# Performance work log

Hardware: AMD Instinct MI355X
Metric: run time of the kernel (lower is better)

The kernel has to match this reference:

```python
import jax, jax.numpy as jnp
import numpy as np
from jax import lax

T, B, DX, H, DZ = 512, 64, 128, 256, 64
W_SCALE = 0.05


def setup_inputs() -> dict:
    key = jax.random.key(0)
    ks = jax.random.split(key, 16)
    r = lambda k, shape, s=W_SCALE: jax.random.normal(k, shape, dtype=jnp.float32) * s
    return {
        "X": jax.random.normal(ks[0], (T, B, DX), dtype=jnp.float32),
        "Wih_f": r(ks[1], (H, DX)), "Whh_f": r(ks[2], (H, H)),
        "bih_f": r(ks[3], (H,)), "bhh_f": r(ks[4], (H,)),
        "Wih_b": r(ks[5], (H, DX)), "Whh_b": r(ks[6], (H, H)),
        "bih_b": r(ks[7], (H,)), "bhh_b": r(ks[8], (H,)),
        "Wt": r(ks[9], (H, DZ)), "bt": r(ks[10], (H,)),
        "Wmu": r(ks[11], (DZ, H)), "bmu": r(ks[12], (DZ,)),
        "Wsig": r(ks[13], (DZ, H)), "bsig": r(ks[14], (DZ,)),
        "eps": jax.random.normal(ks[15], (T, B, DZ), dtype=jnp.float32),
    }


def _rnn_dir(X, Wih, Whh, bih, bhh):
    # Elman RNN (tanh): h_t = tanh(x_t Wih^T + bih + h_{t-1} Whh^T + bhh)
    xproj = jnp.einsum('tbd,hd->tbh', X, Wih) + bih + bhh  # big GEMM hoisted out of scan

    def step(h, xp):
        h = jnp.tanh(xp + h @ Whh.T)
        return h, h

    h0 = jnp.zeros((X.shape[1], Whh.shape[0]), dtype=X.dtype)
    _, hs = lax.scan(step, h0, xproj)
    return hs  # [T,B,H]


def reference(X, Wih_f, Whh_f, bih_f, bhh_f, Wih_b, Whh_b, bih_b, bhh_b,
              Wt, bt, Wmu, bmu, Wsig, bsig, eps):
    h_left = _rnn_dir(X, Wih_f, Whh_f, bih_f, bhh_f)
    h_right = _rnn_dir(X[::-1], Wih_b, Whh_b, bih_b, bhh_b)[::-1]

    def step(z_prev, inputs):
        hl, hr, eps_t = inputs
        tmp = jnp.tanh(z_prev @ Wt.T + bt)           # transition_net
        h_t = (tmp + hl + hr) * (1.0 / 3.0)
        mu = h_t @ Wmu.T + bmu
        std = jax.nn.softplus(h_t @ Wsig.T + bsig)
        z = mu + std * eps_t                         # reparameterization
        return z, (z, mu, std)

    z0 = jnp.zeros((X.shape[1], Wt.shape[1]), dtype=X.dtype)
    _, (z, mu, std) = lax.scan(step, z0, (h_left, h_right, eps))
    # stack outputs {z_post, mu_post, std_post} into one array [3,T,B,DZ]
    return jnp.stack([z, mu, std])
```

## Files before the change

### kernel.cpp

```cpp
#include <hip/hip_runtime.h>

#define TT 512
#define BB 64
#define DXX 128
#define HH 256
#define DZZ 64

typedef __attribute__((ext_vector_type(8))) short short8;
typedef __attribute__((ext_vector_type(4))) float f32x4;

#define DEV static __device__ __forceinline__

DEV unsigned short f2bf(float f){
  unsigned u = __builtin_bit_cast(unsigned, f);
  u += 0x7FFFu + ((u >> 16) & 1u);
  return (unsigned short)(u >> 16);
}
DEV float bf2f(unsigned short s){
  unsigned u = ((unsigned)s) << 16;
  return __builtin_bit_cast(float, u);
}
DEV float ftanh(float x){
  float a = fabsf(x);
  float e = __expf(-2.f * a);
  float r = __builtin_amdgcn_rcpf(1.f + e);
  float t = (1.f - e) * r;
  return copysignf(t, x);
}
DEV float fsoftplus(float x){
  float e = __expf(fminf(x, 20.f));
  float s = __logf(1.f + e);
  return (x > 20.f) ? x : s;
}
DEV short8 pack8(const float* p){
  short8 v;
  #pragma unroll
  for (int i = 0; i < 8; ++i) v[i] = (short)f2bf(p[i]);
  return v;
}


__global__ __launch_bounds__(256, 2) void phaseA(
    const float* __restrict__ X,
    const float* __restrict__ WihF, const float* __restrict__ bihF, const float* __restrict__ bhhF,
    const float* __restrict__ WihB, const float* __restrict__ bihB, const float* __restrict__ bhhB,
    unsigned short* __restrict__ xpF)
{
  const int bid = blockIdx.x;
  const int d = bid >> 9, s = bid & 511;
  const int ts = d ? (TT - 1 - s) : s;
  const float* W  = d ? WihB : WihF;
  const float* bi = d ? bihB : bihF;
  const float* bh = d ? bhhB : bhhF;

  const int tid = threadIdx.x, q = tid >> 6, l = tid & 63;
  const int l15 = l & 15, l4 = l >> 4;

  short8 bfv[4][4];
  float bias[4];
  #pragma unroll
  for (int ni = 0; ni < 4; ++ni){
    int n = 64*q + 16*ni + l15;
    bias[ni] = bi[n] + bh[n];
    #pragma unroll
    for (int ks = 0; ks < 4; ++ks)
      bfv[ni][ks] = pack8(W + (size_t)n * DXX + ks*32 + l4*8);
  }

  #pragma unroll
  for (int bq = 0; bq < 4; ++bq){
    const float* xr = X + ((size_t)ts * 64 + 16*bq + l15) * DXX;
    short8 af[4];
    #pragma unroll
    for (int ks = 0; ks < 4; ++ks) af[ks] = pack8(xr + ks*32 + l4*8);

    f32x4 acc[4];
    #pragma unroll
    for (int ni = 0; ni < 4; ++ni){
      acc[ni][0]=bias[ni]; acc[ni][1]=bias[ni]; acc[ni][2]=bias[ni]; acc[ni][3]=bias[ni];
    }
    #pragma unroll
    for (int ks = 0; ks < 4; ++ks)
      #pragma unroll
      for (int ni = 0; ni < 4; ++ni)
        acc[ni] = __builtin_amdgcn_mfma_f32_16x16x32_bf16(af[ks], bfv[ni][ks], acc[ni], 0, 0, 0);

    unsigned wd[8];
    #pragma unroll
    for (int w8 = 0; w8 < 8; ++w8){
      int ni = w8 >> 1, rb = (w8 & 1) * 2;
      wd[w8] = (unsigned)f2bf(acc[ni][rb]) | ((unsigned)f2bf(acc[ni][rb+1]) << 16);
    }
    unsigned short* dst = xpF + ((((size_t)d*TT + s)*4 + bq)*4 + q)*1024 + (size_t)l*16;
    uint4 o0 = {wd[0], wd[1], wd[2], wd[3]};
    uint4 o1 = {wd[4], wd[5], wd[6], wd[7]};
    ((uint4*)dst)[0] = o0;
    ((uint4*)dst)[1] = o1;
  }
}

__global__ void epsPerm(const float* __restrict__ eps, float* __restrict__ epsF){
  const int t = blockIdx.x, tid = threadIdx.x;
  const int q = tid >> 6, l = tid & 63;
  const int l15 = l & 15, l4 = l >> 4;
  const int nz = 16*q + l15;
  #pragma unroll
  for (int bq = 0; bq < 4; ++bq){
    float4 o;
    int m0 = 16*bq + l4*4;
    o.x = eps[((size_t)t*64 + m0 + 0)*64 + nz];
    o.y = eps[((size_t)t*64 + m0 + 1)*64 + nz];
    o.z = eps[((size_t)t*64 + m0 + 2)*64 + nz];
    o.w = eps[((size_t)t*64 + m0 + 3)*64 + nz];
    *(float4*)(epsF + ((((size_t)t*4 + bq)*4 + q)*64 + l)*4) = o;
  }
}

__global__ __launch_bounds__(256, 1) void phaseB(
    const float* __restrict__ WhhF, const float* __restrict__ WhhB,
    const unsigned short* __restrict__ xpF, unsigned short* __restrict__ hF)
{
  const int dir = blockIdx.x >> 2, bq = blockIdx.x & 3;
  const float* Whh = dir ? WhhB : WhhF;
  const int tid = threadIdx.x, q = tid >> 6, l = tid & 63;
  const int l15 = l & 15, l4 = l >> 4;

  __shared__ __attribute__((aligned(16))) unsigned short hbuf[2][16 * 256];

  short8 bf[4][8];
  #pragma unroll
  for (int ni = 0; ni < 4; ++ni){
    int n = 64*q + 16*ni + l15;
    #pragma unroll
    for (int ks = 0; ks < 8; ++ks)
      bf[ni][ks] = pack8(Whh + (size_t)n * HH + ks*32 + l4*8);
  }
  for (int i = tid; i < 16*256/2; i += 256) ((unsigned*)hbuf[0])[i] = 0u;

  const size_t strideS = 16384;
  const size_t laneOff = (size_t)bq*4096 + (size_t)q*1024 + (size_t)l*16;
  const unsigned short* xpP = xpF + (size_t)dir*TT*strideS + laneOff;
  unsigned short* hD = hF + (size_t)dir*TT*strideS + laneOff;

  uint4 xq0, xq1;
  { const uint4* src = (const uint4*)xpP; xq0 = src[0]; xq1 = src[1]; }

  unsigned pw[8];
  size_t prevOff = 0;
  __syncthreads();

  for (int s = 0; s < TT; ++s){
    if (s > 0){
      uint4 o0 = {pw[0], pw[1], pw[2], pw[3]};
      uint4 o1 = {pw[4], pw[5], pw[6], pw[7]};
      *(uint4*)(hD + prevOff)     = o0;
      *(uint4*)(hD + prevOff + 8) = o1;
    }
    const int rp = s & 1, wc = rp ^ 1;

    f32x4 acc[4];
    {
      unsigned w8v[8] = {xq0.x, xq0.y, xq0.z, xq0.w, xq1.x, xq1.y, xq1.z, xq1.w};
      #pragma unroll
      for (int w8 = 0; w8 < 8; ++w8){
        int ni = w8 >> 1, rb = (w8 & 1) * 2;
        acc[ni][rb]   = bf2f((unsigned short)(w8v[w8] & 0xffff));
        acc[ni][rb+1] = bf2f((unsigned short)(w8v[w8] >> 16));
      }
    }
    if (s + 1 < TT){
      const uint4* src = (const uint4*)(xpP + (size_t)(s+1) * strideS);
      xq0 = src[0]; xq1 = src[1];
    }
    #pragma unroll
    for (int ks = 0; ks < 8; ++ks){
      int idx = (l15*256 + ks*32 + l4*8) ^ ((l15 & 7) << 3);
      short8 a = *(const short8*)(hbuf[rp] + idx);
      #pragma unroll
      for (int ni = 0; ni < 4; ++ni)
        acc[ni] = __builtin_amdgcn_mfma_f32_16x16x32_bf16(a, bf[ni][ks], acc[ni], 0, 0, 0);
    }
    #pragma unroll
    for (int ni = 0; ni < 4; ++ni){
      int n = 64*q + 16*ni + l15;
      #pragma unroll
      for (int rb = 0; rb < 4; rb += 2){
        unsigned u0 = f2bf(ftanh(acc[ni][rb]));
        unsigned u1 = f2bf(ftanh(acc[ni][rb+1]));
        int m0 = l4*4 + rb, m1 = m0 + 1;
        hbuf[wc][(m0*256 + n) ^ ((m0 & 7) << 3)] = (unsigned short)u0;
        hbuf[wc][(m1*256 + n) ^ ((m1 & 7) << 3)] = (unsigned short)u1;
        pw[ni*2 + (rb >> 1)] = u0 | (u1 << 16);
      }
    }
    prevOff = (size_t)(dir ? (TT - 1 - s) : s) * strideS;
    __syncthreads();
  }
  {
    uint4 o0 = {pw[0], pw[1], pw[2], pw[3]};
    uint4 o1 = {pw[4], pw[5], pw[6], pw[7]};
    *(uint4*)(hD + prevOff)     = o0;
    *(uint4*)(hD + prevOff + 8) = o1;
  }
}

__global__ __launch_bounds__(256, 1) void phaseC(
    const float* __restrict__ Wt,  const float* __restrict__ bt,
    const float* __restrict__ Wmu, const float* __restrict__ bmu,
    const float* __restrict__ Wsig,const float* __restrict__ bsig,
    const float* __restrict__ epsF, const unsigned short* __restrict__ hF,
    float* __restrict__ out)
{
  const int bq = blockIdx.x;
  const int tid = threadIdx.x, q = tid >> 6, l = tid & 63;
  const int l15 = l & 15, l4 = l >> 4;

  __shared__ __attribute__((aligned(16))) unsigned short zbuf[16 * 64];
  __shared__ __attribute__((aligned(16))) unsigned short hbuf[16 * 256];

  short8 btf[4][2]; float btr[4];
  #pragma unroll
  for (int ni = 0; ni < 4; ++ni){
    int n = 64*q + 16*ni + l15;
    btr[ni] = bt[n];
    #pragma unroll
    for (int ks = 0; ks < 2; ++ks)
      btf[ni][ks] = pack8(Wt + (size_t)n * DZZ + ks*32 + l4*8);
  }
  short8 bmsf[2][8]; float bms[2];
  {
    int r = 16*q + l15;
    bms[0] = bmu[r]; bms[1] = bsig[r];
    #pragma unroll
    for (int ks = 0; ks < 8; ++ks){
      bmsf[0][ks] = pack8(Wmu  + (size_t)r * HH + ks*32 + l4*8);
      bmsf[1][ks] = pack8(Wsig + (size_t)r * HH + ks*32 + l4*8);
    }
  }
  for (int i = tid; i < 16*64/2; i += 256) ((unsigned*)zbuf)[i] = 0u;

  const size_t strideS = 16384;
  const size_t laneOff = (size_t)bq*4096 + (size_t)q*1024 + (size_t)l*16;
  const unsigned short* hLp = hF + laneOff;
  const unsigned short* hRp = hLp + (size_t)TT * strideS;
  const float* eP = epsF + (((size_t)bq*4 + q)*64 + l)*4;

  unsigned hlw[8], hrw[8];
  float efv[4];
  {
    const uint4* sl = (const uint4*)hLp;
    const uint4* sr = (const uint4*)hRp;
    uint4 a = sl[0], b = sl[1], c = sr[0], d2 = sr[1];
    hlw[0]=a.x; hlw[1]=a.y; hlw[2]=a.z; hlw[3]=a.w; hlw[4]=b.x; hlw[5]=b.y; hlw[6]=b.z; hlw[7]=b.w;
    hrw[0]=c.x; hrw[1]=c.y; hrw[2]=c.z; hrw[3]=c.w; hrw[4]=d2.x; hrw[5]=d2.y; hrw[6]=d2.z; hrw[7]=d2.w;
    float4 e4 = *(const float4*)eP;
    efv[0]=e4.x; efv[1]=e4.y; efv[2]=e4.z; efv[3]=e4.w;
  }
  const size_t TBZ = (size_t)TT * 64 * 64;
  const int nz = 16*q + l15;
  float dmu[4], dsp[4], dz[4];

  __syncthreads();

  for (int t = 0; t < TT; ++t){
    if (t > 0){
      #pragma unroll
      for (int reg = 0; reg < 4; ++reg){
        int M = 16*bq + l4*4 + reg;
        size_t ob = ((size_t)(t-1)*64 + M)*64 + nz;
        out[ob]         = dz[reg];
        out[TBZ + ob]   = dmu[reg];
        out[2*TBZ + ob] = dsp[reg];
      }
    }
    f32x4 at[4];
    #pragma unroll
    for (int ni = 0; ni < 4; ++ni){
      at[ni][0]=btr[ni]; at[ni][1]=btr[ni]; at[ni][2]=btr[ni]; at[ni][3]=btr[ni];
    }
    #pragma unroll
    for (int ks = 0; ks < 2; ++ks){
      int idx = (l15*64 + ks*32 + l4*8) ^ ((l15 & 7) << 3);
      short8 a = *(const short8*)(zbuf + idx);
      #pragma unroll
      for (int ni = 0; ni < 4; ++ni)
        at[ni] = __builtin_amdgcn_mfma_f32_16x16x32_bf16(a, btf[ni][ks], at[ni], 0, 0, 0);
    }
    #pragma unroll
    for (int ni = 0; ni < 4; ++ni){
      int n = 64*q + 16*ni + l15;
      #pragma unroll
      for (int rb = 0; rb < 4; rb += 2){
        unsigned lw = hlw[ni*2 + (rb >> 1)], rw = hrw[ni*2 + (rb >> 1)];
        float h0 = (ftanh(at[ni][rb])   + bf2f((unsigned short)(lw & 0xffff)) + bf2f((unsigned short)(rw & 0xffff))) * (1.f/3.f);
        float h1 = (ftanh(at[ni][rb+1]) + bf2f((unsigned short)(lw >> 16))    + bf2f((unsigned short)(rw >> 16)))    * (1.f/3.f);
        int m0 = l4*4 + rb, m1 = m0 + 1;
        hbuf[(m0*256 + n) ^ ((m0 & 7) << 3)] = f2bf(h0);
        hbuf[(m1*256 + n) ^ ((m1 & 7) << 3)] = f2bf(h1);
      }
    }
    if (t + 1 < TT){
      const uint4* sl = (const uint4*)(hLp + (size_t)(t+1)*strideS);
      const uint4* sr = (const uint4*)(hRp + (size_t)(t+1)*strideS);
      uint4 a = sl[0], b = sl[1], c = sr[0], d2 = sr[1];
      hlw[0]=a.x; hlw[1]=a.y; hlw[2]=a.z; hlw[3]=a.w; hlw[4]=b.x; hlw[5]=b.y; hlw[6]=b.z; hlw[7]=b.w;
      hrw[0]=c.x; hrw[1]=c.y; hrw[2]=c.z; hrw[3]=c.w; hrw[4]=d2.x; hrw[5]=d2.y; hrw[6]=d2.z; hrw[7]=d2.w;
    }
    __syncthreads();

    f32x4 am[2];
    am[0][0]=bms[0]; am[0][1]=bms[0]; am[0][2]=bms[0]; am[0][3]=bms[0];
    am[1][0]=bms[1]; am[1][1]=bms[1]; am[1][2]=bms[1]; am[1][3]=bms[1];
    #pragma unroll
    for (int ks = 0; ks < 8; ++ks){
      int idx = (l15*256 + ks*32 + l4*8) ^ ((l15 & 7) << 3);
      short8 a = *(const short8*)(hbuf + idx);
      am[0] = __builtin_amdgcn_mfma_f32_16x16x32_bf16(a, bmsf[0][ks], am[0], 0, 0, 0);
      am[1] = __builtin_amdgcn_mfma_f32_16x16x32_bf16(a, bmsf[1][ks], am[1], 0, 0, 0);
    }
    #pragma unroll
    for (int reg = 0; reg < 4; ++reg){
      float mu = am[0][reg];
      float sp = fsoftplus(am[1][reg]);
      float zv = mu + sp * efv[reg];
      int m = l4*4 + reg;
      zbuf[(m*64 + nz) ^ ((m & 7) << 3)] = f2bf(zv);
      dmu[reg] = mu; dsp[reg] = sp; dz[reg] = zv;
    }
    if (t + 1 < TT){
      float4 e4 = *(const float4*)(eP + (size_t)(t+1)*4096);
      efv[0]=e4.x; efv[1]=e4.y; efv[2]=e4.z; efv[3]=e4.w;
    }
    __syncthreads();
  }
  {
    #pragma unroll
    for (int reg = 0; reg < 4; ++reg){
      int M = 16*bq + l4*4 + reg;
      size_t ob = ((size_t)(TT-1)*64 + M)*64 + nz;
      out[ob]         = dz[reg];
      out[TBZ + ob]   = dmu[reg];
      out[2*TBZ + ob] = dsp[reg];
    }
  }
}

extern "C" void kernel_launch(void* const* d_in, const int* in_sizes, int n_in,
                              void* d_out, int out_size, void* d_ws, size_t ws_size,
                              hipStream_t stream)
{
  const float* X      = (const float*)d_in[0];
  const float* Wih_f  = (const float*)d_in[1];
  const float* Whh_f  = (const float*)d_in[2];
  const float* bih_f  = (const float*)d_in[3];
  const float* bhh_f  = (const float*)d_in[4];
  const float* Wih_b  = (const float*)d_in[5];
  const float* Whh_b  = (const float*)d_in[6];
  const float* bih_b  = (const float*)d_in[7];
  const float* bhh_b  = (const float*)d_in[8];
  const float* Wt     = (const float*)d_in[9];
  const float* bt     = (const float*)d_in[10];
  const float* Wmu    = (const float*)d_in[11];
  const float* bmu    = (const float*)d_in[12];
  const float* Wsig   = (const float*)d_in[13];
  const float* bsig   = (const float*)d_in[14];
  const float* eps    = (const float*)d_in[15];

  unsigned short* xpF = (unsigned short*)d_ws;
  unsigned short* hF  = xpF + (size_t)2 * TT * 16384;
  float* epsF = (float*)(hF + (size_t)2 * TT * 16384);

  phaseA<<<dim3(1024), dim3(256), 0, stream>>>(X, Wih_f, bih_f, bhh_f, Wih_b, bih_b, bhh_b, xpF);
  epsPerm<<<dim3(512), dim3(256), 0, stream>>>(eps, epsF);
  phaseB<<<dim3(8), dim3(256), 0, stream>>>(Whh_f, Whh_b, xpF, hF);
  phaseC<<<dim3(4), dim3(256), 0, stream>>>(Wt, bt, Wmu, bmu, Wsig, bsig, epsF, hF, (float*)d_out);
}
```

Measured before the change: 1.214 ms.

## Swap MFMA operand order to transpose accumulator layout and drop eps permute kernel

```diff
diff --git a/kernel.cpp b/kernel.cpp
--- a/kernel.cpp
+++ b/kernel.cpp
@@ -16,10 +16,11 @@
   u += 0x7FFFu + ((u >> 16) & 1u);
   return (unsigned short)(u >> 16);
 }
-DEV float bf2f(unsigned short s){
-  unsigned u = ((unsigned)s) << 16;
-  return __builtin_bit_cast(float, u);
-}
+DEV unsigned pack2(float lo, float hi){
+  return (unsigned)f2bf(lo) | ((unsigned)f2bf(hi) << 16);
+}
+DEV float bfLO(unsigned u){ return __builtin_bit_cast(float, u << 16); }
+DEV float bfHI(unsigned u){ return __builtin_bit_cast(float, u & 0xffff0000u); }
 DEV float ftanh(float x){
   float a = fabsf(x);
   float e = __expf(-2.f * a);
@@ -56,63 +57,47 @@
   const int tid = threadIdx.x, q = tid >> 6, l = tid & 63;
   const int l15 = l & 15, l4 = l >> 4;
 
-  short8 bfv[4][4];
-  float bias[4];
+  short8 wf[4][4];
+  f32x4 bias[4];
   #pragma unroll
   for (int ni = 0; ni < 4; ++ni){
     int n = 64*q + 16*ni + l15;
-    bias[ni] = bi[n] + bh[n];
     #pragma unroll
     for (int ks = 0; ks < 4; ++ks)
-      bfv[ni][ks] = pack8(W + (size_t)n * DXX + ks*32 + l4*8);
+      wf[ni][ks] = pack8(W + (size_t)n * DXX + ks*32 + l4*8);
+    int n0 = 64*q + 16*ni + 4*l4;
+    float4 b1 = *(const float4*)(bi + n0);
+    float4 b2 = *(const float4*)(bh + n0);
+    bias[ni][0]=b1.x+b2.x; bias[ni][1]=b1.y+b2.y; bias[ni][2]=b1.z+b2.z; bias[ni][3]=b1.w+b2.w;
   }
 
   #pragma unroll
   for (int bq = 0; bq < 4; ++bq){
     const float* xr = X + ((size_t)ts * 64 + 16*bq + l15) * DXX;
-    short8 af[4];
-    #pragma unroll
-    for (int ks = 0; ks < 4; ++ks) af[ks] = pack8(xr + ks*32 + l4*8);
+    short8 xf[4];
+    #pragma unroll
+    for (int ks = 0; ks < 4; ++ks) xf[ks] = pack8(xr + ks*32 + l4*8);
 
     f32x4 acc[4];
     #pragma unroll
+    for (int ni = 0; ni < 4; ++ni) acc[ni] = bias[ni];
+    #pragma unroll
+    for (int ks = 0; ks < 4; ++ks)
+      #pragma unroll
+      for (int ni = 0; ni < 4; ++ni)
+        acc[ni] = __builtin_amdgcn_mfma_f32_16x16x32_bf16(wf[ni][ks], xf[ks], acc[ni], 0, 0, 0);
+
+    unsigned wd[8];
+    #pragma unroll
     for (int ni = 0; ni < 4; ++ni){
-      acc[ni][0]=bias[ni]; acc[ni][1]=bias[ni]; acc[ni][2]=bias[ni]; acc[ni][3]=bias[ni];
-    }
-    #pragma unroll
-    for (int ks = 0; ks < 4; ++ks)
-      #pragma unroll
-      for (int ni = 0; ni < 4; ++ni)
-        acc[ni] = __builtin_amdgcn_mfma_f32_16x16x32_bf16(af[ks], bfv[ni][ks], acc[ni], 0, 0, 0);
-
-    unsigned wd[8];
-    #pragma unroll
-    for (int w8 = 0; w8 < 8; ++w8){
-      int ni = w8 >> 1, rb = (w8 & 1) * 2;
-      wd[w8] = (unsigned)f2bf(acc[ni][rb]) | ((unsigned)f2bf(acc[ni][rb+1]) << 16);
+      wd[ni*2]   = pack2(acc[ni][0], acc[ni][1]);
+      wd[ni*2+1] = pack2(acc[ni][2], acc[ni][3]);
     }
     unsigned short* dst = xpF + ((((size_t)d*TT + s)*4 + bq)*4 + q)*1024 + (size_t)l*16;
     uint4 o0 = {wd[0], wd[1], wd[2], wd[3]};
     uint4 o1 = {wd[4], wd[5], wd[6], wd[7]};
     ((uint4*)dst)[0] = o0;
     ((uint4*)dst)[1] = o1;
-  }
-}
-
-__global__ void epsPerm(const float* __restrict__ eps, float* __restrict__ epsF){
-  const int t = blockIdx.x, tid = threadIdx.x;
-  const int q = tid >> 6, l = tid & 63;
-  const int l15 = l & 15, l4 = l >> 4;
-  const int nz = 16*q + l15;
-  #pragma unroll
-  for (int bq = 0; bq < 4; ++bq){
-    float4 o;
-    int m0 = 16*bq + l4*4;
-    o.x = eps[((size_t)t*64 + m0 + 0)*64 + nz];
-    o.y = eps[((size_t)t*64 + m0 + 1)*64 + nz];
-    o.z = eps[((size_t)t*64 + m0 + 2)*64 + nz];
-    o.w = eps[((size_t)t*64 + m0 + 3)*64 + nz];
-    *(float4*)(epsF + ((((size_t)t*4 + bq)*4 + q)*64 + l)*4) = o;
   }
 }
 
@@ -124,18 +109,20 @@
   const float* Whh = dir ? WhhB : WhhF;
   const int tid = threadIdx.x, q = tid >> 6, l = tid & 63;
   const int l15 = l & 15, l4 = l >> 4;
-
-  __shared__ __attribute__((aligned(16))) unsigned short hbuf[2][16 * 256];
-
-  short8 bf[4][8];
+  const int swz = (l15 & 7) << 3;
+  const int rbase = l15 * 256;
+
+  __shared__ __attribute__((aligned(16))) unsigned short hbuf[2][4096];
+
+  short8 wf[4][8];
   #pragma unroll
   for (int ni = 0; ni < 4; ++ni){
     int n = 64*q + 16*ni + l15;
     #pragma unroll
     for (int ks = 0; ks < 8; ++ks)
-      bf[ni][ks] = pack8(Whh + (size_t)n * HH + ks*32 + l4*8);
-  }
-  for (int i = tid; i < 16*256/2; i += 256) ((unsigned*)hbuf[0])[i] = 0u;
+      wf[ni][ks] = pack8(Whh + (size_t)n * HH + ks*32 + l4*8);
+  }
+  for (int i = tid; i < 2048; i += 256) ((unsigned*)hbuf[0])[i] = 0u;
 
   const size_t strideS = 16384;
   const size_t laneOff = (size_t)bq*4096 + (size_t)q*1024 + (size_t)l*16;
@@ -145,204 +132,201 @@
   uint4 xq0, xq1;
   { const uint4* src = (const uint4*)xpP; xq0 = src[0]; xq1 = src[1]; }
 
-  unsigned pw[8];
+  uint4 p0, p1;
   size_t prevOff = 0;
   __syncthreads();
 
   for (int s = 0; s < TT; ++s){
     if (s > 0){
-      uint4 o0 = {pw[0], pw[1], pw[2], pw[3]};
-      uint4 o1 = {pw[4], pw[5], pw[6], pw[7]};
-      *(uint4*)(hD + prevOff)     = o0;
-      *(uint4*)(hD + prevOff + 8) = o1;
-    }
-    const int rp = s & 1, wc = rp ^ 1;
-
+      *(uint4*)(hD + prevOff)     = p0;
+      *(uint4*)(hD + prevOff + 8) = p1;
+    }
+    uint4 xn0, xn1;
+    {
+      int sn = (s + 1 < TT) ? s + 1 : s;
+      const uint4* src = (const uint4*)(xpP + (size_t)sn * strideS);
+      xn0 = src[0]; xn1 = src[1];
+    }
     f32x4 acc[4];
     {
-      unsigned w8v[8] = {xq0.x, xq0.y, xq0.z, xq0.w, xq1.x, xq1.y, xq1.z, xq1.w};
-      #pragma unroll
-      for (int w8 = 0; w8 < 8; ++w8){
-        int ni = w8 >> 1, rb = (w8 & 1) * 2;
-        acc[ni][rb]   = bf2f((unsigned short)(w8v[w8] & 0xffff));
-        acc[ni][rb+1] = bf2f((unsigned short)(w8v[w8] >> 16));
+      unsigned W8[8] = {xq0.x, xq0.y, xq0.z, xq0.w, xq1.x, xq1.y, xq1.z, xq1.w};
+      #pragma unroll
+      for (int ni = 0; ni < 4; ++ni){
+        acc[ni][0] = bfLO(W8[ni*2]);   acc[ni][1] = bfHI(W8[ni*2]);
+        acc[ni][2] = bfLO(W8[ni*2+1]); acc[ni][3] = bfHI(W8[ni*2+1]);
       }
     }
-    if (s + 1 < TT){
-      const uint4* src = (const uint4*)(xpP + (size_t)(s+1) * strideS);
-      xq0 = src[0]; xq1 = src[1];
-    }
+    const unsigned short* hb = hbuf[s & 1];
     #pragma unroll
     for (int ks = 0; ks < 8; ++ks){
-      int idx = (l15*256 + ks*32 + l4*8) ^ ((l15 & 7) << 3);
-      short8 a = *(const short8*)(hbuf[rp] + idx);
+      short8 b = *(const short8*)(hb + ((rbase + ks*32 + l4*8) ^ swz));
       #pragma unroll
       for (int ni = 0; ni < 4; ++ni)
-        acc[ni] = __builtin_amdgcn_mfma_f32_16x16x32_bf16(a, bf[ni][ks], acc[ni], 0, 0, 0);
-    }
+        acc[ni] = __builtin_amdgcn_mfma_f32_16x16x32_bf16(wf[ni][ks], b, acc[ni], 0, 0, 0);
+    }
+    unsigned short* hw = hbuf[(s & 1) ^ 1];
+    unsigned wd[8];
     #pragma unroll
     for (int ni = 0; ni < 4; ++ni){
-      int n = 64*q + 16*ni + l15;
-      #pragma unroll
-      for (int rb = 0; rb < 4; rb += 2){
-        unsigned u0 = f2bf(ftanh(acc[ni][rb]));
-        unsigned u1 = f2bf(ftanh(acc[ni][rb+1]));
-        int m0 = l4*4 + rb, m1 = m0 + 1;
-        hbuf[wc][(m0*256 + n) ^ ((m0 & 7) << 3)] = (unsigned short)u0;
-        hbuf[wc][(m1*256 + n) ^ ((m1 & 7) << 3)] = (unsigned short)u1;
-        pw[ni*2 + (rb >> 1)] = u0 | (u1 << 16);
-      }
-    }
+      float t0 = ftanh(acc[ni][0]), t1 = ftanh(acc[ni][1]);
+      float t2 = ftanh(acc[ni][2]), t3 = ftanh(acc[ni][3]);
+      unsigned lo = pack2(t0, t1), hi = pack2(t2, t3);
+      wd[ni*2] = lo; wd[ni*2+1] = hi;
+      int ea = rbase + ((64*q + 16*ni + 4*l4) ^ swz);
+      uint2 v; v.x = lo; v.y = hi;
+      *(uint2*)(hw + ea) = v;
+    }
+    p0.x=wd[0]; p0.y=wd[1]; p0.z=wd[2]; p0.w=wd[3];
+    p1.x=wd[4]; p1.y=wd[5]; p1.z=wd[6]; p1.w=wd[7];
     prevOff = (size_t)(dir ? (TT - 1 - s) : s) * strideS;
+    xq0 = xn0; xq1 = xn1;
     __syncthreads();
   }
-  {
-    uint4 o0 = {pw[0], pw[1], pw[2], pw[3]};
-    uint4 o1 = {pw[4], pw[5], pw[6], pw[7]};
-    *(uint4*)(hD + prevOff)     = o0;
-    *(uint4*)(hD + prevOff + 8) = o1;
-  }
+  *(uint4*)(hD + prevOff)     = p0;
+  *(uint4*)(hD + prevOff + 8) = p1;
 }
 
 __global__ __launch_bounds__(256, 1) void phaseC(
     const float* __restrict__ Wt,  const float* __restrict__ bt,
     const float* __restrict__ Wmu, const float* __restrict__ bmu,
     const float* __restrict__ Wsig,const float* __restrict__ bsig,
-    const float* __restrict__ epsF, const unsigned short* __restrict__ hF,
+    const float* __restrict__ eps, const unsigned short* __restrict__ hF,
     float* __restrict__ out)
 {
   const int bq = blockIdx.x;
   const int tid = threadIdx.x, q = tid >> 6, l = tid & 63;
   const int l15 = l & 15, l4 = l >> 4;
-
-  __shared__ __attribute__((aligned(16))) unsigned short zbuf[16 * 64];
-  __shared__ __attribute__((aligned(16))) unsigned short hbuf[16 * 256];
-
-  short8 btf[4][2]; float btr[4];
+  const int swz = (l15 & 7) << 3;
+  const int rbase = l15 * 256;
+  const int zrbase = l15 * 64;
+
+  __shared__ __attribute__((aligned(16))) unsigned short zbuf[1024];
+  __shared__ __attribute__((aligned(16))) unsigned short hbuf[4096];
+
+  short8 wtf[4][2]; f32x4 btb[4];
   #pragma unroll
   for (int ni = 0; ni < 4; ++ni){
     int n = 64*q + 16*ni + l15;
-    btr[ni] = bt[n];
     #pragma unroll
     for (int ks = 0; ks < 2; ++ks)
-      btf[ni][ks] = pack8(Wt + (size_t)n * DZZ + ks*32 + l4*8);
-  }
-  short8 bmsf[2][8]; float bms[2];
+      wtf[ni][ks] = pack8(Wt + (size_t)n * DZZ + ks*32 + l4*8);
+    float4 b4 = *(const float4*)(bt + 64*q + 16*ni + 4*l4);
+    btb[ni][0]=b4.x; btb[ni][1]=b4.y; btb[ni][2]=b4.z; btb[ni][3]=b4.w;
+  }
+  short8 wm[8], wsg[8];
   {
     int r = 16*q + l15;
-    bms[0] = bmu[r]; bms[1] = bsig[r];
     #pragma unroll
     for (int ks = 0; ks < 8; ++ks){
-      bmsf[0][ks] = pack8(Wmu  + (size_t)r * HH + ks*32 + l4*8);
-      bmsf[1][ks] = pack8(Wsig + (size_t)r * HH + ks*32 + l4*8);
-    }
-  }
-  for (int i = tid; i < 16*64/2; i += 256) ((unsigned*)zbuf)[i] = 0u;
+      wm[ks]  = pack8(Wmu  + (size_t)r * HH + ks*32 + l4*8);
+      wsg[ks] = pack8(Wsig + (size_t)r * HH + ks*32 + l4*8);
+    }
+  }
+  f32x4 bm4, bs4;
+  {
+    float4 a = *(const float4*)(bmu  + 16*q + 4*l4);
+    float4 b = *(const float4*)(bsig + 16*q + 4*l4);
+    bm4[0]=a.x; bm4[1]=a.y; bm4[2]=a.z; bm4[3]=a.w;
+    bs4[0]=b.x; bs4[1]=b.y; bs4[2]=b.z; bs4[3]=b.w;
+  }
+  for (int i = tid; i < 512; i += 256) ((unsigned*)zbuf)[i] = 0u;
 
   const size_t strideS = 16384;
   const size_t laneOff = (size_t)bq*4096 + (size_t)q*1024 + (size_t)l*16;
   const unsigned short* hLp = hF + laneOff;
   const unsigned short* hRp = hLp + (size_t)TT * strideS;
-  const float* eP = epsF + (((size_t)bq*4 + q)*64 + l)*4;
-
-  unsigned hlw[8], hrw[8];
-  float efv[4];
+  const float* eP = eps + ((size_t)(16*bq + l15)) * 64 + 16*q + 4*l4;
+
+  uint4 hl0, hl1, hr0, hr1; f32x4 ef;
   {
     const uint4* sl = (const uint4*)hLp;
     const uint4* sr = (const uint4*)hRp;
-    uint4 a = sl[0], b = sl[1], c = sr[0], d2 = sr[1];
-    hlw[0]=a.x; hlw[1]=a.y; hlw[2]=a.z; hlw[3]=a.w; hlw[4]=b.x; hlw[5]=b.y; hlw[6]=b.z; hlw[7]=b.w;
-    hrw[0]=c.x; hrw[1]=c.y; hrw[2]=c.z; hrw[3]=c.w; hrw[4]=d2.x; hrw[5]=d2.y; hrw[6]=d2.z; hrw[7]=d2.w;
+    hl0 = sl[0]; hl1 = sl[1]; hr0 = sr[0]; hr1 = sr[1];
     float4 e4 = *(const float4*)eP;
-    efv[0]=e4.x; efv[1]=e4.y; efv[2]=e4.z; efv[3]=e4.w;
+    ef[0]=e4.x; ef[1]=e4.y; ef[2]=e4.z; ef[3]=e4.w;
   }
   const size_t TBZ = (size_t)TT * 64 * 64;
-  const int nz = 16*q + l15;
-  float dmu[4], dsp[4], dz[4];
-
+  f32x4 dz, dmu, dsp;
+  size_t obPrev = 0;
   __syncthreads();
 
   for (int t = 0; t < TT; ++t){
     if (t > 0){
-      #pragma unroll
-      for (int reg = 0; reg < 4; ++reg){
-        int M = 16*bq + l4*4 + reg;
-        size_t ob = ((size_t)(t-1)*64 + M)*64 + nz;
-        out[ob]         = dz[reg];
-        out[TBZ + ob]   = dmu[reg];
-        out[2*TBZ + ob] = dsp[reg];
+      *(float4*)(out + obPrev)         = *(float4*)&dz;
+      *(float4*)(out + TBZ + obPrev)   = *(float4*)&dmu;
+      *(float4*)(out + 2*TBZ + obPrev) = *(float4*)&dsp;
+    }
+    uint4 nl0, nl1, nr0, nr1; f32x4 nef;
+    {
+      int tn = (t + 1 < TT) ? t + 1 : t;
+      const uint4* sl = (const uint4*)(hLp + (size_t)tn*strideS);
+      const uint4* sr = (const uint4*)(hRp + (size_t)tn*strideS);
+      nl0 = sl[0]; nl1 = sl[1]; nr0 = sr[0]; nr1 = sr[1];
+      float4 e4 = *(const float4*)(eP + (size_t)tn*4096);
+      nef[0]=e4.x; nef[1]=e4.y; nef[2]=e4.z; nef[3]=e4.w;
+    }
+    f32x4 at[4];
+    #pragma unroll
+    for (int ni = 0; ni < 4; ++ni) at[ni] = btb[ni];
+    #pragma unroll
+    for (int ks = 0; ks < 2; ++ks){
+      short8 b = *(const short8*)(zbuf + ((zrbase + ks*32 + l4*8) ^ swz));
+      #pragma unroll
+      for (int ni = 0; ni < 4; ++ni)
+        at[ni] = __builtin_amdgcn_mfma_f32_16x16x32_bf16(wtf[ni][ks], b, at[ni], 0, 0, 0);
+    }
+    {
+      unsigned HL[8] = {hl0.x, hl0.y, hl0.z, hl0.w, hl1.x, hl1.y, hl1.z, hl1.w};
+      unsigned HR[8] = {hr0.x, hr0.y, hr0.z, hr0.w, hr1.x, hr1.y, hr1.z, hr1.w};
+      #pragma unroll
+      for (int ni = 0; ni < 4; ++ni){
+        unsigned wl0 = HL[ni*2], wl1 = HL[ni*2+1];
+        unsigned wr0 = HR[ni*2], wr1 = HR[ni*2+1];
+        float h0 = (ftanh(at[ni][0]) + bfLO(wl0) + bfLO(wr0)) * (1.f/3.f);
+        float h1 = (ftanh(at[ni][1]) + bfHI(wl0) + bfHI(wr0)) * (1.f/3.f);
+        float h2 = (ftanh(at[ni][2]) + bfLO(wl1) + bfLO(wr1)) * (1.f/3.f);
+        float h3 = (ftanh(at[ni][3]) + bfHI(wl1) + bfHI(wr1)) * (1.f/3.f);
+        int ea = rbase + ((64*q + 16*ni + 4*l4) ^ swz);
+        uint2 v; v.x = pack2(h0, h1); v.y = pack2(h2, h3);
+        *(uint2*)(hbuf + ea) = v;
       }
     }
-    f32x4 at[4];
-    #pragma unroll
-    for (int ni = 0; ni < 4; ++ni){
-      at[ni][0]=btr[ni]; at[ni][1]=btr[ni]; at[ni][2]=btr[ni]; at[ni][3]=btr[ni];
-    }
-    #pragma unroll
-    for (int ks = 0; ks < 2; ++ks){
-      int idx = (l15*64 + ks*32 + l4*8) ^ ((l15 & 7) << 3);
-      short8 a = *(const short8*)(zbuf + idx);
-      #pragma unroll
-      for (int ni = 0; ni < 4; ++ni)
-        at[ni] = __builtin_amdgcn_mfma_f32_16x16x32_bf16(a, btf[ni][ks], at[ni], 0, 0, 0);
-    }
-    #pragma unroll
-    for (int ni = 0; ni < 4; ++ni){
-      int n = 64*q + 16*ni + l15;
-      #pragma unroll
-      for (int rb = 0; rb < 4; rb += 2){
-        unsigned lw = hlw[ni*2 + (rb >> 1)], rw = hrw[ni*2 + (rb >> 1)];
-        float h0 = (ftanh(at[ni][rb])   + bf2f((unsigned short)(lw & 0xffff)) + bf2f((unsigned short)(rw & 0xffff))) * (1.f/3.f);
-        float h1 = (ftanh(at[ni][rb+1]) + bf2f((unsigned short)(lw >> 16))    + bf2f((unsigned short)(rw >> 16)))    * (1.f/3.f);
-        int m0 = l4*4 + rb, m1 = m0 + 1;
-        hbuf[(m0*256 + n) ^ ((m0 & 7) << 3)] = f2bf(h0);
-        hbuf[(m1*256 + n) ^ ((m1 & 7) << 3)] = f2bf(h1);
-      }
-    }
-    if (t + 1 < TT){
-      const uint4* sl = (const uint4*)(hLp + (size_t)(t+1)*strideS);
-      const uint4* sr = (const uint4*)(hRp + (size_t)(t+1)*strideS);
-      uint4 a = sl[0], b = sl[1], c = sr[0], d2 = sr[1];
-      hlw[0]=a.x; hlw[1]=a.y; hlw[2]=a.z; hlw[3]=a.w; hlw[4]=b.x; hlw[5]=b.y; hlw[6]=b.z; hlw[7]=b.w;
-      hrw[0]=c.x; hrw[1]=c.y; hrw[2]=c.z; hrw[3]=c.w; hrw[4]=d2.x; hrw[5]=d2.y; hrw[6]=d2.z; hrw[7]=d2.w;
-    }
     __syncthreads();
 
-    f32x4 am[2];
-    am[0][0]=bms[0]; am[0][1]=bms[0]; am[0][2]=bms[0]; am[0][3]=bms[0];
-    am[1][0]=bms[1]; am[1][1]=bms[1]; am[1][2]=bms[1]; am[1][3]=bms[1];
-    #pragma unroll
-    for (int ks = 0; ks < 8; ++ks){
-      int idx = (l15*256 + ks*32 + l4*8) ^ ((l15 & 7) << 3);
-      short8 a = *(const short8*)(hbuf + idx);
-      am[0] = __builtin_amdgcn_mfma_f32_16x16x32_bf16(a, bmsf[0][ks], am[0], 0, 0, 0);
-      am[1] = __builtin_amdgcn_mfma_f32_16x16x32_bf16(a, bmsf[1][ks], am[1], 0, 0, 0);
-    }
+    f32x4 a0 = bm4, s0 = bs4;
+    f32x4 a1 = {0.f,0.f,0.f,0.f}, s1 = {0.f,0.f,0.f,0.f};
+    #pragma unroll
+    for (int ks = 0; ks < 4; ++ks){
+      short8 b = *(const short8*)(hbuf + ((rbase + ks*32 + l4*8) ^ swz));
+      a0 = __builtin_amdgcn_mfma_f32_16x16x32_bf16(wm[ks],  b, a0, 0, 0, 0);
+      s0 = __builtin_amdgcn_mfma_f32_16x16x32_bf16(wsg[ks], b, s0, 0, 0, 0);
+    }
+    #pragma unroll
+    for (int ks = 4; ks < 8; ++ks){
+      short8 b = *(const short8*)(hbuf + ((rbase + ks*32 + l4*8) ^ swz));
+      a1 = __builtin_amdgcn_mfma_f32_16x16x32_bf16(wm[ks],  b, a1, 0, 0, 0);
+      s1 = __builtin_amdgcn_mfma_f32_16x16x32_bf16(wsg[ks], b, s1, 0, 0, 0);
+    }
+    f32x4 mu = a0 + a1;
+    f32x4 sg = s0 + s1;
     #pragma unroll
     for (int reg = 0; reg < 4; ++reg){
-      float mu = am[0][reg];
-      float sp = fsoftplus(am[1][reg]);
-      float zv = mu + sp * efv[reg];
-      int m = l4*4 + reg;
-      zbuf[(m*64 + nz) ^ ((m & 7) << 3)] = f2bf(zv);
-      dmu[reg] = mu; dsp[reg] = sp; dz[reg] = zv;
-    }
-    if (t + 1 < TT){
-      float4 e4 = *(const float4*)(eP + (size_t)(t+1)*4096);
-      efv[0]=e4.x; efv[1]=e4.y; efv[2]=e4.z; efv[3]=e4.w;
-    }
+      float sp = fsoftplus(sg[reg]);
+      float zv = __builtin_fmaf(sp, ef[reg], mu[reg]);
+      dz[reg] = zv; dmu[reg] = mu[reg]; dsp[reg] = sp;
+    }
+    {
+      int zea = zrbase + ((16*q + 4*l4) ^ swz);
+      uint2 v; v.x = pack2(dz[0], dz[1]); v.y = pack2(dz[2], dz[3]);
+      *(uint2*)(zbuf + zea) = v;
+    }
+    obPrev = ((size_t)t*64 + 16*bq + l15)*64 + 16*q + 4*l4;
+    hl0 = nl0; hl1 = nl1; hr0 = nr0; hr1 = nr1; ef = nef;
     __syncthreads();
   }
-  {
-    #pragma unroll
-    for (int reg = 0; reg < 4; ++reg){
-      int M = 16*bq + l4*4 + reg;
-      size_t ob = ((size_t)(TT-1)*64 + M)*64 + nz;
-      out[ob]         = dz[reg];
-      out[TBZ + ob]   = dmu[reg];
-      out[2*TBZ + ob] = dsp[reg];
-    }
-  }
+  *(float4*)(out + obPrev)         = *(float4*)&dz;
+  *(float4*)(out + TBZ + obPrev)   = *(float4*)&dmu;
+  *(float4*)(out + 2*TBZ + obPrev) = *(float4*)&dsp;
 }
 
 extern "C" void kernel_launch(void* const* d_in, const int* in_sizes, int n_in,
@@ -368,10 +352,8 @@
 
   unsigned short* xpF = (unsigned short*)d_ws;
   unsigned short* hF  = xpF + (size_t)2 * TT * 16384;
-  float* epsF = (float*)(hF + (size_t)2 * TT * 16384);
 
   phaseA<<<dim3(1024), dim3(256), 0, stream>>>(X, Wih_f, bih_f, bhh_f, Wih_b, bih_b, bhh_b, xpF);
-  epsPerm<<<dim3(512), dim3(256), 0, stream>>>(eps, epsF);
   phaseB<<<dim3(8), dim3(256), 0, stream>>>(Whh_f, Whh_b, xpF, hF);
-  phaseC<<<dim3(4), dim3(256), 0, stream>>>(Wt, bt, Wmu, bmu, Wsig, bsig, epsF, hF, (float*)d_out);
-}
+  phaseC<<<dim3(4), dim3(256), 0, stream>>>(Wt, bt, Wmu, bmu, Wsig, bsig, eps, hF, (float*)d_out);
+}
```

Measured after the change: 1.272 ms. +4.8%, slower.
